# Kernel optimization log

Hardware: AMD Instinct MI355X
Metric: run time of the kernel (lower is better)

The kernel has to match this reference:

```python
import jax, jax.numpy as jnp
import numpy as np

N, FIN, H, C, D = 50000, 128, 4, 64, 4
E = 800000


def leaky_relu(x, slope):
    return jnp.where(x >= 0, x, slope * x)


def gat_layer(x, src, dst, W, A, att_src, att_dst, bias):
    # x: [N, Fin]; W: [Fin, H*C]; A: [Fin, H*D]; att_*: [H, D]; bias: [C]
    n = x.shape[0]
    h = (x @ W).reshape(n, H, -1)          # [N, H, C] message features
    a = (x @ A).reshape(n, H, -1)          # [N, H, D] attention features
    alpha_src = jnp.einsum('nhd,hd->nh', a, att_src)   # [N, H]
    alpha_dst = jnp.einsum('nhd,hd->nh', a, att_dst)   # [N, H]
    e = leaky_relu(alpha_src[src] + alpha_dst[dst], 0.2)  # [E, H]
    # edge softmax over incoming edges of each destination node
    m = jax.ops.segment_max(e, dst, num_segments=n)       # [N, H]
    ex = jnp.exp(e - m[dst])                               # [E, H]
    denom = jax.ops.segment_sum(ex, dst, num_segments=n)  # [N, H]
    w = ex / denom[dst]                                    # [E, H]
    msg = h[src] * w[..., None]                            # [E, H, C]
    out = jax.ops.segment_sum(msg, dst, num_segments=n)   # [N, H, C]
    return out.mean(axis=1) + bias                         # head-average -> [N, C]


def setup_inputs() -> dict:
    key = jax.random.key(0)
    ks = jax.random.split(key, 12)
    x = jax.random.normal(ks[0], (N, FIN), dtype=jnp.float32)
    edge_index = jax.random.randint(ks[1], (2, E), 0, N, dtype=jnp.int64)
    s = 0.05
    return {
        'x': x,
        'edge_index': edge_index,
        'W1': jax.random.normal(ks[2], (FIN, H * C), dtype=jnp.float32) * s,
        'A1': jax.random.normal(ks[3], (FIN, H * D), dtype=jnp.float32) * s,
        'att_src1': jax.random.normal(ks[4], (H, D), dtype=jnp.float32) * s,
        'att_dst1': jax.random.normal(ks[5], (H, D), dtype=jnp.float32) * s,
        'b1': jnp.zeros((C,), dtype=jnp.float32),
        'W2': jax.random.normal(ks[6], (C, H * C), dtype=jnp.float32) * s,
        'A2': jax.random.normal(ks[7], (C, H * D), dtype=jnp.float32) * s,
        'att_src2': jax.random.normal(ks[8], (H, D), dtype=jnp.float32) * s,
        'att_dst2': jax.random.normal(ks[9], (H, D), dtype=jnp.float32) * s,
        'b2': jnp.zeros((C,), dtype=jnp.float32),
    }


def reference(x, edge_index, W1, A1, att_src1, att_dst1, b1, W2, A2, att_src2, att_dst2, b2):
    src, dst = edge_index[0], edge_index[1]
    x = gat_layer(x, src, dst, W1, A1, att_src1, att_dst1, b1)
    x = leaky_relu(x, 0.1)
    x = gat_layer(x, src, dst, W2, A2, att_src2, att_dst2, b2)
    x = leaky_relu(x, 0.1)
    return x
```

## Files before the change

kernel.cpp:

```cpp
#include <hip/hip_runtime.h>


#define N_NODES 50000
#define N_EDGES 800000
#define NB_SCAN 196

typedef _Float16 half4 __attribute__((ext_vector_type(4)));
typedef __attribute__((ext_vector_type(8))) short short8;
typedef __attribute__((ext_vector_type(4))) float f32x4;
typedef __attribute__((ext_vector_type(8))) unsigned short ushort8;

__device__ __forceinline__ float bf2f(unsigned short u){
  return __uint_as_float(((unsigned int)u) << 16);
}
__device__ __forceinline__ unsigned short f2bf(float f){
  unsigned int u = __float_as_uint(f);
  u = (u + 0x7FFFu + ((u >> 16) & 1u)) >> 16;
  return (unsigned short)u;
}
__device__ __forceinline__ float ldf(const void* p, int i, bool bf){
  return bf ? bf2f(((const unsigned short*)p)[i]) : ((const float*)p)[i];
}

__global__ void k_detect(const unsigned int* __restrict__ xb, int* __restrict__ flag){
  int l = threadIdx.x;
  unsigned int w = xb[l] & 0xFFFFu;
  unsigned int e = (w >> 7) & 0xFFu;
  bool hit = (e >= 100u && e <= 135u);
  unsigned long long m = __ballot(hit);
  if (l == 0) *flag = (__popcll(m) > 40) ? 1 : 0;
}

struct SetupPtrs {
  const void *W1, *A1, *aS1, *aD1, *b1, *W2, *A2, *aS2, *aD2, *b2;
};

__global__ __launch_bounds__(256) void k_setup(SetupPtrs S,
    int* __restrict__ deg, int* __restrict__ fill,
    unsigned short* __restrict__ Wb1, unsigned short* __restrict__ Wb2,
    unsigned short* __restrict__ Bsd1f, unsigned short* __restrict__ Bsd2f,
    float* __restrict__ bc1, float* __restrict__ bc2,
    const int* __restrict__ flag)
{
  const bool bf = (*flag != 0);
  const int b = blockIdx.x, tid = threadIdx.x;
  if (b < 196){
    int i = b * 256 + tid;
    if (i < N_NODES){ deg[i] = 0; fill[i] = 0; }
  } else if (b < 324){
    int t = (b - 196) * 256 + tid;
    int j = t & 7, lane = (t >> 3) & 63, kt = (t >> 9) & 3, nt = t >> 11;
    int k = kt * 32 + (lane >> 4) * 8 + j;
    int n = nt * 16 + (lane & 15);
    Wb1[t] = bf ? ((const unsigned short*)S.W1)[k * 256 + n]
                : f2bf(((const float*)S.W1)[k * 256 + n]);
  } else if (b < 388){
    int t = (b - 324) * 256 + tid;
    int j = t & 7, lane = (t >> 3) & 63, kt = (t >> 9) & 1, nt = t >> 10;
    int k = kt * 32 + (lane >> 4) * 8 + j;
    int n = nt * 16 + (lane & 15);
    Wb2[t] = bf ? ((const unsigned short*)S.W2)[k * 256 + n]
                : f2bf(((const float*)S.W2)[k * 256 + n]);
  } else if (b < 396){
    int t = (b - 388) * 256 + tid;
    int j = t & 7, lane = (t >> 3) & 63, kt = t >> 9;
    int k = kt * 32 + (lane >> 4) * 8 + j;
    int c = lane & 15;
    float v = 0.f;
    if (c < 4){
      for (int dd = 0; dd < 4; ++dd)
        v += ldf(S.A1, k * 16 + c * 4 + dd, bf) * ldf(S.aS1, c * 4 + dd, bf);
    } else if (c < 8){
      int h = c - 4;
      for (int dd = 0; dd < 4; ++dd)
        v += ldf(S.A1, k * 16 + h * 4 + dd, bf) * ldf(S.aD1, h * 4 + dd, bf);
    }
    Bsd1f[t] = f2bf(v);
  } else if (b < 400){
    int t = (b - 396) * 256 + tid;
    int j = t & 7, lane = (t >> 3) & 63, kt = t >> 9;
    int k = kt * 32 + (lane >> 4) * 8 + j;
    int c = lane & 15;
    float v = 0.f;
    if (c < 4){
      for (int dd = 0; dd < 4; ++dd)
        v += ldf(S.A2, k * 16 + c * 4 + dd, bf) * ldf(S.aS2, c * 4 + dd, bf);
    } else if (c < 8){
      int h = c - 4;
      for (int dd = 0; dd < 4; ++dd)
        v += ldf(S.A2, k * 16 + h * 4 + dd, bf) * ldf(S.aD2, h * 4 + dd, bf);
    }
    Bsd2f[t] = f2bf(v);
  } else {
    if (tid < 64)       bc1[tid] = ldf(S.b1, tid, bf);
    else if (tid < 128) bc2[tid - 64] = ldf(S.b2, tid - 64, bf);
  }
}


__global__ __launch_bounds__(256) void k_hist(const int* __restrict__ dst,
                                              int* __restrict__ deg){
  int e = blockIdx.x * 256 + threadIdx.x;
  if (e < N_EDGES) atomicAdd(&deg[dst[e]], 1);
}

__global__ __launch_bounds__(256) void k_scan1(const int* __restrict__ deg,
                                               int* __restrict__ blocksum){
  int b = blockIdx.x, t = threadIdx.x, i = b * 256 + t;
  int v = (i < N_NODES) ? deg[i] : 0;
  for (int off = 1; off < 64; off <<= 1) v += __shfl_xor(v, off);
  __shared__ int sm[4];
  if ((t & 63) == 0) sm[t >> 6] = v;
  __syncthreads();
  if (t == 0) blocksum[b] = sm[0] + sm[1] + sm[2] + sm[3];
}

__global__ __launch_bounds__(256) void k_scan23(const int* __restrict__ deg,
                                                const int* __restrict__ blocksum,
                                                int* __restrict__ rowptr){
  __shared__ int sb[256];
  __shared__ int sm[256];
  int b = blockIdx.x, t = threadIdx.x, i = b * 256 + t;
  int vb = (t < NB_SCAN) ? blocksum[t] : 0;
  sb[t] = vb;
  int v = (i < N_NODES) ? deg[i] : 0;
  sm[t] = v;
  __syncthreads();
  for (int off = 1; off < 256; off <<= 1){
    int ub = (t >= off) ? sb[t - off] : 0;
    int um = (t >= off) ? sm[t - off] : 0;
    __syncthreads();
    sb[t] += ub; sm[t] += um;
    __syncthreads();
  }
  int blockoff = (b > 0) ? sb[b - 1] : 0;
  if (i < N_NODES) rowptr[i] = blockoff + sm[t] - v;
  if (i == 0) rowptr[N_NODES] = N_EDGES;
}

__global__ __launch_bounds__(256) void k_scatter(const int* __restrict__ src,
                                                 const int* __restrict__ dst,
                                                 const int* __restrict__ rowptr,
                                                 int* __restrict__ fill,
                                                 int* __restrict__ csr_src){
  int e = blockIdx.x * 256 + threadIdx.x;
  if (e < N_EDGES){
    int d = dst[e];
    int pos = rowptr[d] + atomicAdd(&fill[d], 1);
    csr_src[pos] = src[e];
  }
}


template<int F, bool DYN>
__global__ __launch_bounds__(256) void k_nodeM(const void* __restrict__ xin_,
    const unsigned short* __restrict__ Wb, const unsigned short* __restrict__ Bsdf,
    _Float16* __restrict__ hmat, float* __restrict__ alpha_s, float* __restrict__ alpha_d,
    const int* __restrict__ flag)
{
  const int STR = F + 8;
  const int KT  = F / 32;
  const int CH  = F / 8;
  __shared__ unsigned short xs[64 * (F + 8)];
  const int tid = threadIdx.x;
  const int base = blockIdx.x * 64;
  bool bf = true;
  if (DYN) bf = (*flag != 0);
  for (int v = tid; v < 64 * CH; v += 256){
    int row = v / CH, c8 = v % CH;
    int node = base + row; if (node >= N_NODES) node = N_NODES - 1;
    size_t g = (size_t)node * F + c8 * 8;
    ushort8 u;
    if (!DYN || bf){
      u = *(const ushort8*)((const unsigned short*)xin_ + g);
    } else {
      const float* xf = (const float*)xin_ + g;
      float4 f0 = *(const float4*)xf, f1 = *(const float4*)(xf + 4);
      u[0]=f2bf(f0.x); u[1]=f2bf(f0.y); u[2]=f2bf(f0.z); u[3]=f2bf(f0.w);
      u[4]=f2bf(f1.x); u[5]=f2bf(f1.y); u[6]=f2bf(f1.z); u[7]=f2bf(f1.w);
    }
    *(ushort8*)&xs[row * STR + c8 * 8] = u;
  }
  __syncthreads();

  const int wave = tid >> 6, l = tid & 63;
  const int quad = l >> 4, m = l & 15;
  const int wbase = base + wave * 16;

  short8 afrag[KT];
  #pragma unroll
  for (int kt = 0; kt < KT; ++kt)
    afrag[kt] = *(const short8*)&xs[(wave * 16 + m) * STR + kt * 32 + quad * 8];

  f32x4 aacc = (f32x4)0.f;
  #pragma unroll
  for (int kt = 0; kt < KT; ++kt){
    short8 sdfrag = *(const short8*)(Bsdf + ((size_t)kt * 64 + l) * 8);
    aacc = __builtin_amdgcn_mfma_f32_16x16x32_bf16(afrag[kt], sdfrag, aacc, 0, 0, 0);
  }
  if (m < 8){
    float* dstp = (m < 4) ? alpha_s : alpha_d;
    int hh = m & 3;
    #pragma unroll
    for (int r = 0; r < 4; ++r){
      int node = wbase + quad * 4 + r;
      if (node < N_NODES) dstp[node * 4 + hh] = aacc[r];
    }
  }

  f32x4 acc[16];
  #pragma unroll
  for (int nt = 0; nt < 16; ++nt) acc[nt] = (f32x4)0.f;

  #pragma unroll
  for (int nt = 0; nt < 16; ++nt){
    #pragma unroll
    for (int kt = 0; kt < KT; ++kt){
      short8 bfrag = *(const short8*)(Wb + ((size_t)(nt * KT + kt) * 64 + l) * 8);
      acc[nt] = __builtin_amdgcn_mfma_f32_16x16x32_bf16(afrag[kt], bfrag, acc[nt], 0, 0, 0);
    }
  }
  #pragma unroll
  for (int r = 0; r < 4; ++r){
    int node = wbase + quad * 4 + r;
    if (node < N_NODES){
      #pragma unroll
      for (int nt = 0; nt < 16; ++nt)
        hmat[(size_t)node * 256 + nt * 16 + m] = (_Float16)acc[nt][r];
    }
  }
}


template<int MODE>
__global__ __launch_bounds__(256) void k_aggr(
    const _Float16* __restrict__ hmat, const float* __restrict__ alpha_s,
    const float* __restrict__ alpha_d, const int* __restrict__ rowptr,
    const int* __restrict__ csr_src, const float* __restrict__ bias,
    void* __restrict__ out, const int* __restrict__ flag)
{
  const int tid = threadIdx.x;
  const int wave = tid >> 6, l = tid & 63;
  const int n = blockIdx.x * 4 + wave;
  const int hh = l >> 4;
  const float adv = alpha_d[n * 4 + hh];
  const int p0 = rowptr[n], p1 = rowptr[n + 1];
  const char* hb = (const char*)hmat + l * 8;
  const char* ab = (const char*)alpha_s + hh * 4;
  float4 acc = make_float4(0.f,0.f,0.f,0.f);
  float den = 0.f;
  int p = p0;
  int pa = (p0 + 3) & ~3; if (pa > p1) pa = p1;
  for (; p < pa; ++p){
    int s = csr_src[p];
    float e = *(const float*)(ab + ((unsigned)s << 4)) + adv;
    e = fmaxf(e, 0.2f * e);
    float ex = __expf(e);
    half4 hv = *(const half4*)(hb + ((unsigned)s << 9));
    den += ex;
    acc.x += ex * (float)hv.x; acc.y += ex * (float)hv.y;
    acc.z += ex * (float)hv.z; acc.w += ex * (float)hv.w;
  }
  for (; p + 4 <= p1; p += 4){
    int4 s4 = *(const int4*)(csr_src + p);
    float a0 = *(const float*)(ab + ((unsigned)s4.x << 4));
    float a1 = *(const float*)(ab + ((unsigned)s4.y << 4));
    float a2 = *(const float*)(ab + ((unsigned)s4.z << 4));
    float a3 = *(const float*)(ab + ((unsigned)s4.w << 4));
    half4 h0 = *(const half4*)(hb + ((unsigned)s4.x << 9));
    half4 h1 = *(const half4*)(hb + ((unsigned)s4.y << 9));
    half4 h2 = *(const half4*)(hb + ((unsigned)s4.z << 9));
    half4 h3 = *(const half4*)(hb + ((unsigned)s4.w << 9));
    float e0 = a0 + adv; e0 = fmaxf(e0, 0.2f * e0);
    float e1 = a1 + adv; e1 = fmaxf(e1, 0.2f * e1);
    float e2 = a2 + adv; e2 = fmaxf(e2, 0.2f * e2);
    float e3 = a3 + adv; e3 = fmaxf(e3, 0.2f * e3);
    float ex0 = __expf(e0), ex1 = __expf(e1), ex2 = __expf(e2), ex3 = __expf(e3);
    den += (ex0 + ex1) + (ex2 + ex3);
    acc.x += ex0 * (float)h0.x + ex1 * (float)h1.x + ex2 * (float)h2.x + ex3 * (float)h3.x;
    acc.y += ex0 * (float)h0.y + ex1 * (float)h1.y + ex2 * (float)h2.y + ex3 * (float)h3.y;
    acc.z += ex0 * (float)h0.z + ex1 * (float)h1.z + ex2 * (float)h2.z + ex3 * (float)h3.z;
    acc.w += ex0 * (float)h0.w + ex1 * (float)h1.w + ex2 * (float)h2.w + ex3 * (float)h3.w;
  }
  for (; p < p1; ++p){
    int s = csr_src[p];
    float e = *(const float*)(ab + ((unsigned)s << 4)) + adv;
    e = fmaxf(e, 0.2f * e);
    float ex = __expf(e);
    half4 hv = *(const half4*)(hb + ((unsigned)s << 9));
    den += ex;
    acc.x += ex * (float)hv.x; acc.y += ex * (float)hv.y;
    acc.z += ex * (float)hv.z; acc.w += ex * (float)hv.w;
  }
  float r = (den > 0.f) ? (1.f / den) : 0.f;
  acc.x *= r; acc.y *= r; acc.z *= r; acc.w *= r;
  acc.x += __shfl_xor(acc.x, 16); acc.y += __shfl_xor(acc.y, 16);
  acc.z += __shfl_xor(acc.z, 16); acc.w += __shfl_xor(acc.w, 16);
  acc.x += __shfl_xor(acc.x, 32); acc.y += __shfl_xor(acc.y, 32);
  acc.z += __shfl_xor(acc.z, 32); acc.w += __shfl_xor(acc.w, 32);
  if (l < 16){
    float vx = 0.25f * acc.x + bias[l * 4 + 0];
    float vy = 0.25f * acc.y + bias[l * 4 + 1];
    float vz = 0.25f * acc.z + bias[l * 4 + 2];
    float vw = 0.25f * acc.w + bias[l * 4 + 3];
    vx = fmaxf(vx, 0.1f * vx);
    vy = fmaxf(vy, 0.1f * vy);
    vz = fmaxf(vz, 0.1f * vz);
    vw = fmaxf(vw, 0.1f * vw);
    if (MODE == 0){
      ushort4 o = make_ushort4(f2bf(vx), f2bf(vy), f2bf(vz), f2bf(vw));
      *(ushort4*)((unsigned short*)out + (size_t)n * 64 + l * 4) = o;
    } else {
      if (*flag){
        ushort4 o = make_ushort4(f2bf(vx), f2bf(vy), f2bf(vz), f2bf(vw));
        *(ushort4*)((unsigned short*)out + (size_t)n * 64 + l * 4) = o;
      } else {
        *(float4*)((float*)out + (size_t)n * 64 + l * 4) = make_float4(vx, vy, vz, vw);
      }
    }
  }
}


extern "C" void kernel_launch(void* const* d_in, const int* in_sizes, int n_in,
                              void* d_out, int out_size, void* d_ws, size_t ws_size,
                              hipStream_t stream)
{
  const void* x  = d_in[0];
  const int* ei  = (const int*)d_in[1];
  const int* src = ei;
  const int* dst = ei + N_EDGES;

  char* ws = (char*)d_ws;
  _Float16* hmat = (_Float16*)(ws);
  unsigned short* Wb1 = (unsigned short*)(ws + 25600000);
  unsigned short* Wb2 = (unsigned short*)(ws + 25665536);
  unsigned short* x2  = (unsigned short*)(ws + 51200000);
  float* as_    = (float*)(ws + 64000000);
  float* ad_    = (float*)(ws + 64800000);
  int*   deg    = (int*)  (ws + 65600000);
  int*   fill   = (int*)  (ws + 65800000);
  int*   rowptr = (int*)  (ws + 66000000);
  int*   csr    = (int*)  (ws + 66200064);
  int*   flag   = (int*)  (ws + 69400064);
  float* bc1    = (float*)(ws + 69539520);
  float* bc2    = (float*)(ws + 69609536);
  int*   bsum   = (int*)  (ws + 69609792);
  unsigned short* Bsd1f = (unsigned short*)(ws + 69611840);
  unsigned short* Bsd2f = (unsigned short*)(ws + 69615936);

  k_detect<<<1, 64, 0, stream>>>((const unsigned int*)x, flag);

  SetupPtrs S;
  S.W1 = d_in[2];  S.A1 = d_in[3];  S.aS1 = d_in[4];  S.aD1 = d_in[5];  S.b1 = d_in[6];
  S.W2 = d_in[7];  S.A2 = d_in[8];  S.aS2 = d_in[9];  S.aD2 = d_in[10]; S.b2 = d_in[11];
  k_setup<<<401, 256, 0, stream>>>(S, deg, fill, Wb1, Wb2,
                                   Bsd1f, Bsd2f, bc1, bc2, flag);

  k_hist   <<<(N_EDGES + 255) / 256, 256, 0, stream>>>(dst, deg);
  k_scan1  <<<NB_SCAN, 256, 0, stream>>>(deg, bsum);
  k_scan23 <<<NB_SCAN, 256, 0, stream>>>(deg, bsum, rowptr);
  k_scatter<<<(N_EDGES + 255) / 256, 256, 0, stream>>>(src, dst, rowptr, fill, csr);

  k_nodeM<128, true><<<(N_NODES + 63) / 64, 256, 0, stream>>>(x, Wb1, Bsd1f, hmat, as_, ad_, flag);
  k_aggr<0><<<N_NODES / 4, 256, 0, stream>>>(hmat, as_, ad_, rowptr, csr, bc1, x2, flag);
  k_nodeM<64, false><<<(N_NODES + 63) / 64, 256, 0, stream>>>(x2, Wb2, Bsd2f, hmat, as_, ad_, flag);
  k_aggr<1><<<N_NODES / 4, 256, 0, stream>>>(hmat, as_, ad_, rowptr, csr, bc2, d_out, flag);
}
```

Before: 336.3 us.

## Inline dtype detection, seed fill from rowptr, swap MFMA operands for vector stores

Removes the separate k_detect launch by recomputing the bf16/f32 dtype check inside each kernel with a wave ballot. The scan kernel now also writes rowptr into the fill array, so scatter needs a single atomic per edge and no rowptr read, and setup no longer zeroes fill. In k_nodeM the MFMA operands are swapped so each lane holds four consecutive output columns for one node. Alpha and hmat stores then become float4/half4 vector writes instead of scalar scattered ones. The cost is redundant per-block detection loads of x's first words.

After: 353.2 us. 5.0% more time.

```diff
diff --git a/kernel.cpp b/kernel.cpp
--- a/kernel.cpp
+++ b/kernel.cpp
@@ -22,13 +22,12 @@
   return bf ? bf2f(((const unsigned short*)p)[i]) : ((const float*)p)[i];
 }
 
-__global__ void k_detect(const unsigned int* __restrict__ xb, int* __restrict__ flag){
-  int l = threadIdx.x;
-  unsigned int w = xb[l] & 0xFFFFu;
+__device__ __forceinline__ bool detect_bf(const unsigned int* __restrict__ xb, int tid){
+  unsigned int w = xb[tid & 63] & 0xFFFFu;
   unsigned int e = (w >> 7) & 0xFFu;
   bool hit = (e >= 100u && e <= 135u);
   unsigned long long m = __ballot(hit);
-  if (l == 0) *flag = (__popcll(m) > 40) ? 1 : 0;
+  return __popcll(m) > 40;
 }
 
 struct SetupPtrs {
@@ -36,17 +35,17 @@
 };
 
 __global__ __launch_bounds__(256) void k_setup(SetupPtrs S,
-    int* __restrict__ deg, int* __restrict__ fill,
+    const unsigned int* __restrict__ xb,
+    int* __restrict__ deg,
     unsigned short* __restrict__ Wb1, unsigned short* __restrict__ Wb2,
     unsigned short* __restrict__ Bsd1f, unsigned short* __restrict__ Bsd2f,
-    float* __restrict__ bc1, float* __restrict__ bc2,
-    const int* __restrict__ flag)
+    float* __restrict__ bc1, float* __restrict__ bc2)
 {
-  const bool bf = (*flag != 0);
   const int b = blockIdx.x, tid = threadIdx.x;
+  const bool bf = detect_bf(xb, tid);
   if (b < 196){
     int i = b * 256 + tid;
-    if (i < N_NODES){ deg[i] = 0; fill[i] = 0; }
+    if (i < N_NODES) deg[i] = 0;
   } else if (b < 324){
     int t = (b - 196) * 256 + tid;
     int j = t & 7, lane = (t >> 3) & 63, kt = (t >> 9) & 3, nt = t >> 11;
@@ -117,7 +116,8 @@
 
 __global__ __launch_bounds__(256) void k_scan23(const int* __restrict__ deg,
                                                 const int* __restrict__ blocksum,
-                                                int* __restrict__ rowptr){
+                                                int* __restrict__ rowptr,
+                                                int* __restrict__ fill){
   __shared__ int sb[256];
   __shared__ int sm[256];
   int b = blockIdx.x, t = threadIdx.x, i = b * 256 + t;
@@ -134,19 +134,21 @@
     __syncthreads();
   }
   int blockoff = (b > 0) ? sb[b - 1] : 0;
-  if (i < N_NODES) rowptr[i] = blockoff + sm[t] - v;
+  if (i < N_NODES){
+    int rp = blockoff + sm[t] - v;
+    rowptr[i] = rp;
+    fill[i]   = rp;
+  }
   if (i == 0) rowptr[N_NODES] = N_EDGES;
 }
 
 __global__ __launch_bounds__(256) void k_scatter(const int* __restrict__ src,
                                                  const int* __restrict__ dst,
-                                                 const int* __restrict__ rowptr,
                                                  int* __restrict__ fill,
                                                  int* __restrict__ csr_src){
   int e = blockIdx.x * 256 + threadIdx.x;
   if (e < N_EDGES){
-    int d = dst[e];
-    int pos = rowptr[d] + atomicAdd(&fill[d], 1);
+    int pos = atomicAdd(&fill[dst[e]], 1);
     csr_src[pos] = src[e];
   }
 }
@@ -154,9 +156,9 @@
 
 template<int F, bool DYN>
 __global__ __launch_bounds__(256) void k_nodeM(const void* __restrict__ xin_,
+    const unsigned int* __restrict__ xb,
     const unsigned short* __restrict__ Wb, const unsigned short* __restrict__ Bsdf,
-    _Float16* __restrict__ hmat, float* __restrict__ alpha_s, float* __restrict__ alpha_d,
-    const int* __restrict__ flag)
+    _Float16* __restrict__ hmat, float* __restrict__ alpha_s, float* __restrict__ alpha_d)
 {
   const int STR = F + 8;
   const int KT  = F / 32;
@@ -165,7 +167,7 @@
   const int tid = threadIdx.x;
   const int base = blockIdx.x * 64;
   bool bf = true;
-  if (DYN) bf = (*flag != 0);
+  if (DYN) bf = detect_bf(xb, tid);
   for (int v = tid; v < 64 * CH; v += 256){
     int row = v / CH, c8 = v % CH;
     int node = base + row; if (node >= N_NODES) node = N_NODES - 1;
@@ -186,26 +188,24 @@
   const int wave = tid >> 6, l = tid & 63;
   const int quad = l >> 4, m = l & 15;
   const int wbase = base + wave * 16;
-
-  short8 afrag[KT];
+  const int node = wbase + m;
+
+  short8 xfrag[KT];
   #pragma unroll
   for (int kt = 0; kt < KT; ++kt)
-    afrag[kt] = *(const short8*)&xs[(wave * 16 + m) * STR + kt * 32 + quad * 8];
+    xfrag[kt] = *(const short8*)&xs[(wave * 16 + m) * STR + kt * 32 + quad * 8];
 
   f32x4 aacc = (f32x4)0.f;
   #pragma unroll
   for (int kt = 0; kt < KT; ++kt){
     short8 sdfrag = *(const short8*)(Bsdf + ((size_t)kt * 64 + l) * 8);
-    aacc = __builtin_amdgcn_mfma_f32_16x16x32_bf16(afrag[kt], sdfrag, aacc, 0, 0, 0);
-  }
-  if (m < 8){
-    float* dstp = (m < 4) ? alpha_s : alpha_d;
-    int hh = m & 3;
-    #pragma unroll
-    for (int r = 0; r < 4; ++r){
-      int node = wbase + quad * 4 + r;
-      if (node < N_NODES) dstp[node * 4 + hh] = aacc[r];
-    }
+    aacc = __builtin_amdgcn_mfma_f32_16x16x32_bf16(sdfrag, xfrag[kt], aacc, 0, 0, 0);
+  }
+  if (node < N_NODES){
+    if (quad == 0)
+      *(float4*)(alpha_s + node * 4) = make_float4(aacc[0], aacc[1], aacc[2], aacc[3]);
+    else if (quad == 1)
+      *(float4*)(alpha_d + node * 4) = make_float4(aacc[0], aacc[1], aacc[2], aacc[3]);
   }
 
   f32x4 acc[16];
@@ -216,17 +216,17 @@
   for (int nt = 0; nt < 16; ++nt){
     #pragma unroll
     for (int kt = 0; kt < KT; ++kt){
-      short8 bfrag = *(const short8*)(Wb + ((size_t)(nt * KT + kt) * 64 + l) * 8);
-      acc[nt] = __builtin_amdgcn_mfma_f32_16x16x32_bf16(afrag[kt], bfrag, acc[nt], 0, 0, 0);
-    }
-  }
-  #pragma unroll
-  for (int r = 0; r < 4; ++r){
-    int node = wbase + quad * 4 + r;
-    if (node < N_NODES){
-      #pragma unroll
-      for (int nt = 0; nt < 16; ++nt)
-        hmat[(size_t)node * 256 + nt * 16 + m] = (_Float16)acc[nt][r];
+      short8 wfrag = *(const short8*)(Wb + ((size_t)(nt * KT + kt) * 64 + l) * 8);
+      acc[nt] = __builtin_amdgcn_mfma_f32_16x16x32_bf16(wfrag, xfrag[kt], acc[nt], 0, 0, 0);
+    }
+  }
+  if (node < N_NODES){
+    #pragma unroll
+    for (int nt = 0; nt < 16; ++nt){
+      half4 o;
+      o.x = (_Float16)acc[nt][0]; o.y = (_Float16)acc[nt][1];
+      o.z = (_Float16)acc[nt][2]; o.w = (_Float16)acc[nt][3];
+      *(half4*)(hmat + (size_t)node * 256 + nt * 16 + quad * 4) = o;
     }
   }
 }
@@ -237,9 +237,11 @@
     const _Float16* __restrict__ hmat, const float* __restrict__ alpha_s,
     const float* __restrict__ alpha_d, const int* __restrict__ rowptr,
     const int* __restrict__ csr_src, const float* __restrict__ bias,
-    void* __restrict__ out, const int* __restrict__ flag)
+    void* __restrict__ out, const unsigned int* __restrict__ xb)
 {
   const int tid = threadIdx.x;
+  bool bfout = true;
+  if (MODE == 1) bfout = detect_bf(xb, tid);
   const int wave = tid >> 6, l = tid & 63;
   const int n = blockIdx.x * 4 + wave;
   const int hh = l >> 4;
@@ -307,16 +309,11 @@
     vy = fmaxf(vy, 0.1f * vy);
     vz = fmaxf(vz, 0.1f * vz);
     vw = fmaxf(vw, 0.1f * vw);
-    if (MODE == 0){
+    if (MODE == 0 || bfout){
       ushort4 o = make_ushort4(f2bf(vx), f2bf(vy), f2bf(vz), f2bf(vw));
       *(ushort4*)((unsigned short*)out + (size_t)n * 64 + l * 4) = o;
     } else {
-      if (*flag){
-        ushort4 o = make_ushort4(f2bf(vx), f2bf(vy), f2bf(vz), f2bf(vw));
-        *(ushort4*)((unsigned short*)out + (size_t)n * 64 + l * 4) = o;
-      } else {
-        *(float4*)((float*)out + (size_t)n * 64 + l * 4) = make_float4(vx, vy, vz, vw);
-      }
+      *(float4*)((float*)out + (size_t)n * 64 + l * 4) = make_float4(vx, vy, vz, vw);
     }
   }
 }
@@ -327,6 +324,7 @@
                               hipStream_t stream)
 {
   const void* x  = d_in[0];
+  const unsigned int* xb = (const unsigned int*)d_in[0];
   const int* ei  = (const int*)d_in[1];
   const int* src = ei;
   const int* dst = ei + N_EDGES;
@@ -342,28 +340,24 @@
   int*   fill   = (int*)  (ws + 65800000);
   int*   rowptr = (int*)  (ws + 66000000);
   int*   csr    = (int*)  (ws + 66200064);
-  int*   flag   = (int*)  (ws + 69400064);
   float* bc1    = (float*)(ws + 69539520);
   float* bc2    = (float*)(ws + 69609536);
   int*   bsum   = (int*)  (ws + 69609792);
   unsigned short* Bsd1f = (unsigned short*)(ws + 69611840);
   unsigned short* Bsd2f = (unsigned short*)(ws + 69615936);
 
-  k_detect<<<1, 64, 0, stream>>>((const unsigned int*)x, flag);
-
   SetupPtrs S;
   S.W1 = d_in[2];  S.A1 = d_in[3];  S.aS1 = d_in[4];  S.aD1 = d_in[5];  S.b1 = d_in[6];
   S.W2 = d_in[7];  S.A2 = d_in[8];  S.aS2 = d_in[9];  S.aD2 = d_in[10]; S.b2 = d_in[11];
-  k_setup<<<401, 256, 0, stream>>>(S, deg, fill, Wb1, Wb2,
-                                   Bsd1f, Bsd2f, bc1, bc2, flag);
+  k_setup<<<401, 256, 0, stream>>>(S, xb, deg, Wb1, Wb2, Bsd1f, Bsd2f, bc1, bc2);
 
   k_hist   <<<(N_EDGES + 255) / 256, 256, 0, stream>>>(dst, deg);
   k_scan1  <<<NB_SCAN, 256, 0, stream>>>(deg, bsum);
-  k_scan23 <<<NB_SCAN, 256, 0, stream>>>(deg, bsum, rowptr);
-  k_scatter<<<(N_EDGES + 255) / 256, 256, 0, stream>>>(src, dst, rowptr, fill, csr);
-
-  k_nodeM<128, true><<<(N_NODES + 63) / 64, 256, 0, stream>>>(x, Wb1, Bsd1f, hmat, as_, ad_, flag);
-  k_aggr<0><<<N_NODES / 4, 256, 0, stream>>>(hmat, as_, ad_, rowptr, csr, bc1, x2, flag);
-  k_nodeM<64, false><<<(N_NODES + 63) / 64, 256, 0, stream>>>(x2, Wb2, Bsd2f, hmat, as_, ad_, flag);
-  k_aggr<1><<<N_NODES / 4, 256, 0, stream>>>(hmat, as_, ad_, rowptr, csr, bc2, d_out, flag);
-}
+  k_scan23 <<<NB_SCAN, 256, 0, stream>>>(deg, bsum, rowptr, fill);
+  k_scatter<<<(N_EDGES + 255) / 256, 256, 0, stream>>>(src, dst, fill, csr);
+
+  k_nodeM<128, true><<<(N_NODES + 63) / 64, 256, 0, stream>>>(x, xb, Wb1, Bsd1f, hmat, as_, ad_);
+  k_aggr<0><<<N_NODES / 4, 256, 0, stream>>>(hmat, as_, ad_, rowptr, csr, bc1, x2, xb);
+  k_nodeM<64, false><<<(N_NODES + 63) / 64, 256, 0, stream>>>(x2, nullptr, Wb2, Bsd2f, hmat, as_, ad_);
+  k_aggr<1><<<N_NODES / 4, 256, 0, stream>>>(hmat, as_, ad_, rowptr, csr, bc2, d_out, xb);
+}
```

## Fuse histogram into setup and CSR scatter into first node GEMM launch

Applied to the files above, without the earlier changes.

Merges the degree histogram into the weight-setup kernel, and the CSR scatter into the layer-1 node transform kernel, using blockIdx ranges so the independent work shares one launch each. Zeroing of deg/fill moves to a hipMemsetAsync. This removes two kernel launches and lets independent work overlap on the GPU, at the cost of heterogeneous blocks and a shared-memory footprint that the scatter blocks reserve but never use. The deg and fill buffers are contiguous, so a single memset covers both.

Result: faster. 326.0 us (-3.1%).

```diff
diff --git a/kernel.cpp b/kernel.cpp
--- a/kernel.cpp
+++ b/kernel.cpp
@@ -4,6 +4,7 @@
 #define N_NODES 50000
 #define N_EDGES 800000
 #define NB_SCAN 196
+#define NB_EDGE 3125
 
 typedef _Float16 half4 __attribute__((ext_vector_type(4)));
 typedef __attribute__((ext_vector_type(8))) short short8;
@@ -35,34 +36,37 @@
   const void *W1, *A1, *aS1, *aD1, *b1, *W2, *A2, *aS2, *aD2, *b2;
 };
 
-__global__ __launch_bounds__(256) void k_setup(SetupPtrs S,
-    int* __restrict__ deg, int* __restrict__ fill,
+__global__ __launch_bounds__(256) void k_setup_hist(SetupPtrs S,
+    const int* __restrict__ dst, int* __restrict__ deg,
     unsigned short* __restrict__ Wb1, unsigned short* __restrict__ Wb2,
     unsigned short* __restrict__ Bsd1f, unsigned short* __restrict__ Bsd2f,
     float* __restrict__ bc1, float* __restrict__ bc2,
     const int* __restrict__ flag)
 {
+  const int b = blockIdx.x, tid = threadIdx.x;
+  if (b < NB_EDGE){
+    int e = b * 256 + tid;
+    if (e < N_EDGES) atomicAdd(&deg[dst[e]], 1);
+    return;
+  }
   const bool bf = (*flag != 0);
-  const int b = blockIdx.x, tid = threadIdx.x;
-  if (b < 196){
-    int i = b * 256 + tid;
-    if (i < N_NODES){ deg[i] = 0; fill[i] = 0; }
-  } else if (b < 324){
-    int t = (b - 196) * 256 + tid;
+  const int bw = b - NB_EDGE;
+  if (bw < 128){
+    int t = bw * 256 + tid;
     int j = t & 7, lane = (t >> 3) & 63, kt = (t >> 9) & 3, nt = t >> 11;
     int k = kt * 32 + (lane >> 4) * 8 + j;
     int n = nt * 16 + (lane & 15);
     Wb1[t] = bf ? ((const unsigned short*)S.W1)[k * 256 + n]
                 : f2bf(((const float*)S.W1)[k * 256 + n]);
-  } else if (b < 388){
-    int t = (b - 324) * 256 + tid;
+  } else if (bw < 192){
+    int t = (bw - 128) * 256 + tid;
     int j = t & 7, lane = (t >> 3) & 63, kt = (t >> 9) & 1, nt = t >> 10;
     int k = kt * 32 + (lane >> 4) * 8 + j;
     int n = nt * 16 + (lane & 15);
     Wb2[t] = bf ? ((const unsigned short*)S.W2)[k * 256 + n]
                 : f2bf(((const float*)S.W2)[k * 256 + n]);
-  } else if (b < 396){
-    int t = (b - 388) * 256 + tid;
+  } else if (bw < 200){
+    int t = (bw - 192) * 256 + tid;
     int j = t & 7, lane = (t >> 3) & 63, kt = t >> 9;
     int k = kt * 32 + (lane >> 4) * 8 + j;
     int c = lane & 15;
@@ -76,8 +80,8 @@
         v += ldf(S.A1, k * 16 + h * 4 + dd, bf) * ldf(S.aD1, h * 4 + dd, bf);
     }
     Bsd1f[t] = f2bf(v);
-  } else if (b < 400){
-    int t = (b - 396) * 256 + tid;
+  } else if (bw < 204){
+    int t = (bw - 200) * 256 + tid;
     int j = t & 7, lane = (t >> 3) & 63, kt = t >> 9;
     int k = kt * 32 + (lane >> 4) * 8 + j;
     int c = lane & 15;
@@ -97,12 +101,6 @@
   }
 }
 
-
-__global__ __launch_bounds__(256) void k_hist(const int* __restrict__ dst,
-                                              int* __restrict__ deg){
-  int e = blockIdx.x * 256 + threadIdx.x;
-  if (e < N_EDGES) atomicAdd(&deg[dst[e]], 1);
-}
 
 __global__ __launch_bounds__(256) void k_scan1(const int* __restrict__ deg,
                                                int* __restrict__ blocksum){
@@ -138,22 +136,10 @@
   if (i == 0) rowptr[N_NODES] = N_EDGES;
 }
 
-__global__ __launch_bounds__(256) void k_scatter(const int* __restrict__ src,
-                                                 const int* __restrict__ dst,
-                                                 const int* __restrict__ rowptr,
-                                                 int* __restrict__ fill,
-                                                 int* __restrict__ csr_src){
-  int e = blockIdx.x * 256 + threadIdx.x;
-  if (e < N_EDGES){
-    int d = dst[e];
-    int pos = rowptr[d] + atomicAdd(&fill[d], 1);
-    csr_src[pos] = src[e];
-  }
-}
-
 
 template<int F, bool DYN>
-__global__ __launch_bounds__(256) void k_nodeM(const void* __restrict__ xin_,
+__device__ __forceinline__ void nodeM_body(int nblk, int tid,
+    const void* __restrict__ xin_,
     const unsigned short* __restrict__ Wb, const unsigned short* __restrict__ Bsdf,
     _Float16* __restrict__ hmat, float* __restrict__ alpha_s, float* __restrict__ alpha_d,
     const int* __restrict__ flag)
@@ -162,8 +148,7 @@
   const int KT  = F / 32;
   const int CH  = F / 8;
   __shared__ unsigned short xs[64 * (F + 8)];
-  const int tid = threadIdx.x;
-  const int base = blockIdx.x * 64;
+  const int base = nblk * 64;
   bool bf = true;
   if (DYN) bf = (*flag != 0);
   for (int v = tid; v < 64 * CH; v += 256){
@@ -229,6 +214,37 @@
         hmat[(size_t)node * 256 + nt * 16 + m] = (_Float16)acc[nt][r];
     }
   }
+}
+
+__global__ __launch_bounds__(256) void k_scatter_node1(
+    const int* __restrict__ src, const int* __restrict__ dst,
+    const int* __restrict__ rowptr, int* __restrict__ fill,
+    int* __restrict__ csr_src,
+    const void* __restrict__ xin_,
+    const unsigned short* __restrict__ Wb, const unsigned short* __restrict__ Bsdf,
+    _Float16* __restrict__ hmat, float* __restrict__ alpha_s, float* __restrict__ alpha_d,
+    const int* __restrict__ flag)
+{
+  const int b = blockIdx.x, tid = threadIdx.x;
+  if (b < NB_EDGE){
+    int e = b * 256 + tid;
+    if (e < N_EDGES){
+      int d = dst[e];
+      int pos = rowptr[d] + atomicAdd(&fill[d], 1);
+      csr_src[pos] = src[e];
+    }
+    return;
+  }
+  nodeM_body<128, true>(b - NB_EDGE, tid, xin_, Wb, Bsdf, hmat, alpha_s, alpha_d, flag);
+}
+
+template<int F, bool DYN>
+__global__ __launch_bounds__(256) void k_nodeM(const void* __restrict__ xin_,
+    const unsigned short* __restrict__ Wb, const unsigned short* __restrict__ Bsdf,
+    _Float16* __restrict__ hmat, float* __restrict__ alpha_s, float* __restrict__ alpha_d,
+    const int* __restrict__ flag)
+{
+  nodeM_body<F, DYN>(blockIdx.x, threadIdx.x, xin_, Wb, Bsdf, hmat, alpha_s, alpha_d, flag);
 }
 
 
@@ -350,19 +366,20 @@
   unsigned short* Bsd2f = (unsigned short*)(ws + 69615936);
 
   k_detect<<<1, 64, 0, stream>>>((const unsigned int*)x, flag);
+  hipMemsetAsync(deg, 0, 2 * N_NODES * sizeof(int), stream);
 
   SetupPtrs S;
   S.W1 = d_in[2];  S.A1 = d_in[3];  S.aS1 = d_in[4];  S.aD1 = d_in[5];  S.b1 = d_in[6];
   S.W2 = d_in[7];  S.A2 = d_in[8];  S.aS2 = d_in[9];  S.aD2 = d_in[10]; S.b2 = d_in[11];
-  k_setup<<<401, 256, 0, stream>>>(S, deg, fill, Wb1, Wb2,
-                                   Bsd1f, Bsd2f, bc1, bc2, flag);
-
-  k_hist   <<<(N_EDGES + 255) / 256, 256, 0, stream>>>(dst, deg);
-  k_scan1  <<<NB_SCAN, 256, 0, stream>>>(deg, bsum);
-  k_scan23 <<<NB_SCAN, 256, 0, stream>>>(deg, bsum, rowptr);
-  k_scatter<<<(N_EDGES + 255) / 256, 256, 0, stream>>>(src, dst, rowptr, fill, csr);
-
-  k_nodeM<128, true><<<(N_NODES + 63) / 64, 256, 0, stream>>>(x, Wb1, Bsd1f, hmat, as_, ad_, flag);
+  k_setup_hist<<<NB_EDGE + 205, 256, 0, stream>>>(S, dst, deg, Wb1, Wb2,
+                                                  Bsd1f, Bsd2f, bc1, bc2, flag);
+
+  k_scan1 <<<NB_SCAN, 256, 0, stream>>>(deg, bsum);
+  k_scan23<<<NB_SCAN, 256, 0, stream>>>(deg, bsum, rowptr);
+
+  k_scatter_node1<<<NB_EDGE + (N_NODES + 63) / 64, 256, 0, stream>>>(
+      src, dst, rowptr, fill, csr, x, Wb1, Bsd1f, hmat, as_, ad_, flag);
+
   k_aggr<0><<<N_NODES / 4, 256, 0, stream>>>(hmat, as_, ad_, rowptr, csr, bc1, x2, flag);
   k_nodeM<64, false><<<(N_NODES + 63) / 64, 256, 0, stream>>>(x2, Wb2, Bsd2f, hmat, as_, ad_, flag);
   k_aggr<1><<<N_NODES / 4, 256, 0, stream>>>(hmat, as_, ad_, rowptr, csr, bc2, d_out, flag);
```
